# Kernel tuning notes

Measured on AMD Instinct MI355X. Metric: run time of the kernel, lower is better.

The kernel has to match this reference:

```python
import jax, jax.numpy as jnp
import numpy as np

T, N, D, L, H = 128, 256, 256, 3, 4


def _ln(x, s, b):
    m = jnp.mean(x, axis=-1, keepdims=True)
    v = jnp.mean((x - m) ** 2, axis=-1, keepdims=True)
    return (x - m) / jnp.sqrt(v + 1e-5) * s + b


def setup_inputs() -> dict:
    key = jax.random.key(0)
    ks = jax.random.split(key, 12)
    s = 0.05
    d = D
    return {
        "spatial_states": jax.random.normal(ks[0], (T, N, d), jnp.float32),
        "re_norm": jax.random.uniform(ks[1], (), jnp.float32),
        "sensor_time": jnp.cumsum(jax.random.uniform(ks[2], (T,), jnp.float32) * 0.1),
        "re_proj_w": jax.random.normal(ks[3], (d, 1), jnp.float32) * s,
        "re_proj_b": jnp.zeros((d,), jnp.float32),
        "tb_n1_s": jnp.ones((d,), jnp.float32),
        "tb_n1_b": jnp.zeros((d,), jnp.float32),
        "tb_in_w": jax.random.normal(ks[4], (3 * d, d), jnp.float32) * s,
        "tb_in_b": jnp.zeros((3 * d,), jnp.float32),
        "tb_out_w": jax.random.normal(ks[5], (d, d), jnp.float32) * s,
        "tb_out_b": jnp.zeros((d,), jnp.float32),
        "tb_n2_s": jnp.ones((d,), jnp.float32),
        "tb_n2_b": jnp.zeros((d,), jnp.float32),
        "tb_ff1_w": jax.random.normal(ks[6], (2 * d, d), jnp.float32) * s,
        "tb_ff1_b": jnp.zeros((2 * d,), jnp.float32),
        "tb_ff2_w": jax.random.normal(ks[7], (d, 2 * d), jnp.float32) * s,
        "tb_ff2_b": jnp.zeros((d,), jnp.float32),
        "cell_ff1_w": jax.random.normal(ks[8], (L, d, 2 * d), jnp.float32) * s,
        "cell_ff1_b": jnp.zeros((L, d), jnp.float32),
        "cell_ff2_w": jax.random.normal(ks[9], (L, d, 2 * d), jnp.float32) * s,
        "cell_ff2_b": jnp.zeros((L, d), jnp.float32),
        "cell_logtau": jnp.tile(jnp.linspace(-1.0, 1.0, d, dtype=jnp.float32), (L, 1)),
        "cell_tb_w": jax.random.normal(ks[10], (L, d, 2 * d), jnp.float32) * s,
        "cell_tb_b": jnp.zeros((L, d), jnp.float32),
    }


def reference(spatial_states, re_norm, sensor_time,
              re_proj_w, re_proj_b,
              tb_n1_s, tb_n1_b, tb_in_w, tb_in_b, tb_out_w, tb_out_b,
              tb_n2_s, tb_n2_b, tb_ff1_w, tb_ff1_b, tb_ff2_w, tb_ff2_b,
              cell_ff1_w, cell_ff1_b, cell_ff2_w, cell_ff2_b,
              cell_logtau, cell_tb_w, cell_tb_b):
    t, n, d = spatial_states.shape
    nL = cell_logtau.shape[0]
    hd = d // H

    # dt per step: first absolute time, then diffs (as in torch source)
    dts = jnp.concatenate([sensor_time[:1], sensor_time[1:] - sensor_time[:-1]])  # [T]
    re_bias = re_proj_w[:, 0] * re_norm + re_proj_b  # [d]

    def token_block(x):  # x: [T, N, d]; attention over N, batched over T
        y = _ln(x, tb_n1_s, tb_n1_b)
        qkv = y @ tb_in_w.T + tb_in_b
        q, k, v = jnp.split(qkv, 3, axis=-1)
        q = q.reshape(t, n, H, hd)
        k = k.reshape(t, n, H, hd)
        v = v.reshape(t, n, H, hd)
        logits = jnp.einsum('bqhd,bkhd->bhqk', q, k) / jnp.sqrt(jnp.float32(hd))
        a = jax.nn.softmax(logits, axis=-1)
        o = jnp.einsum('bhqk,bkhd->bqhd', a, v).reshape(t, n, d)
        x = x + (o @ tb_out_w.T + tb_out_b)
        y = _ln(x, tb_n2_s, tb_n2_b)
        f = jax.nn.silu(y @ tb_ff1_w.T + tb_ff1_b) @ tb_ff2_w.T + tb_ff2_b
        return x + f

    seq = spatial_states
    for l in range(nL):
        # token attention + re_bias are independent of the recurrence -> vectorize over T
        xs = token_block(seq) + re_bias  # [T, N, d]
        w1, b1 = cell_ff1_w[l], cell_ff1_b[l]
        w2, b2 = cell_ff2_w[l], cell_ff2_b[l]
        wt, bt = cell_tb_w[l], cell_tb_b[l]
        tau = jnp.exp(cell_logtau[l])  # [d]

        def step(h, xd):
            x_t, dt = xd
            xh = jnp.concatenate([x_t, h], axis=-1)  # [N, 2d]
            f1 = jnp.tanh(xh @ w1.T + b1)
            f2 = jnp.tanh(xh @ w2.T + b2)
            gate = jax.nn.sigmoid(-tau * dt + (xh @ wt.T + bt))
            h_new = gate * f1 + (1.0 - gate) * f2
            return h_new, h_new

        h0 = jnp.zeros((n, d), seq.dtype)
        _, outs = jax.lax.scan(step, h0, (xs, dts))  # outs: [T, N, d]
        seq = outs + seq if l > 0 else outs
    return seq
```

## Files before the change

kernel.cpp:

```cpp
#include <hip/hip_runtime.h>


#define T_DIM 128
#define N_DIM 256
#define D_DIM 256
#define H_DIM 4
#define HD_DIM 64
#define L_DIM 3
#define TN (T_DIM * N_DIM)

typedef __bf16 bf16x8 __attribute__((ext_vector_type(8)));
typedef __bf16 bf16x4 __attribute__((ext_vector_type(4)));
typedef float f32x4 __attribute__((ext_vector_type(4)));

#define LDS_BAR()                                            \
  do {                                                       \
    asm volatile("s_waitcnt lgkmcnt(0)" ::: "memory");       \
    __builtin_amdgcn_s_barrier();                            \
    __builtin_amdgcn_sched_barrier(0);                       \
  } while (0)

__device__ inline float wave_reduce_sum(float v) {
#pragma unroll
  for (int off = 32; off > 0; off >>= 1) v += __shfl_xor(v, off);
  return v;
}

__device__ inline float bf_to_f(unsigned short u) {
  return __uint_as_float((unsigned int)u << 16);
}

__global__ __launch_bounds__(256) void ln_kernel(const float* __restrict__ x,
                                                 const float* __restrict__ sc,
                                                 const float* __restrict__ bi,
                                                 __bf16* __restrict__ y) {
  const int wid = threadIdx.x >> 6;
  const int lane = threadIdx.x & 63;
  const size_t row = (size_t)blockIdx.x * 4 + wid;
  const float4 xv = *(const float4*)(x + row * D_DIM + lane * 4);
  float s = xv.x + xv.y + xv.z + xv.w;
  float ss = xv.x * xv.x + xv.y * xv.y + xv.z * xv.z + xv.w * xv.w;
  s = wave_reduce_sum(s);
  ss = wave_reduce_sum(ss);
  const float mean = s * (1.f / D_DIM);
  const float var = ss * (1.f / D_DIM) - mean * mean;
  const float r = rsqrtf(var + 1e-5f);
  const float4 scv = *(const float4*)(sc + lane * 4);
  const float4 biv = *(const float4*)(bi + lane * 4);
  bf16x4 ov;
  ov[0] = (__bf16)((xv.x - mean) * r * scv.x + biv.x);
  ov[1] = (__bf16)((xv.y - mean) * r * scv.y + biv.y);
  ov[2] = (__bf16)((xv.z - mean) * r * scv.z + biv.z);
  ov[3] = (__bf16)((xv.w - mean) * r * scv.w + biv.w);
  *(bf16x4*)(y + row * D_DIM + lane * 4) = ov;
}

template <int EPI, int OBF>
__global__ __launch_bounds__(256) void gemm_tiled(const __bf16* __restrict__ A,
                                                  const __bf16* __restrict__ W,
                                                  const float* __restrict__ bias,
                                                  const float* __restrict__ R,
                                                  void* __restrict__ outv,
                                                  int M, int Nout, int K) {
  __shared__ __bf16 a_lds[128][72];
  __shared__ __bf16 b_lds[128][72];
  const int tid = threadIdx.x;
  const int w = tid >> 6, l = tid & 63;
  const int lr = l & 15, kg = l >> 4;
  const int wm = (w & 1) * 64, wn = (w >> 1) * 64;
  const int m0 = blockIdx.x * 128, n0 = blockIdx.y * 128;
  const int srow = tid >> 1, scol = (tid & 1) * 32;
  const __bf16* ag = A + (size_t)(m0 + srow) * K + scol;
  const __bf16* bg = W + (size_t)(n0 + srow) * K + scol;

  bf16x8 av[4], bv[4];
#pragma unroll
  for (int c = 0; c < 4; ++c) {
    av[c] = *(const bf16x8*)(ag + c * 8);
    bv[c] = *(const bf16x8*)(bg + c * 8);
  }

  f32x4 acc[4][4] = {};
  for (int k0 = 0; k0 < K; k0 += 64) {
    LDS_BAR();
#pragma unroll
    for (int c = 0; c < 4; ++c) {
      *(bf16x8*)&a_lds[srow][scol + c * 8] = av[c];
      *(bf16x8*)&b_lds[srow][scol + c * 8] = bv[c];
    }
    if (k0 + 64 < K) {
#pragma unroll
      for (int c = 0; c < 4; ++c) {
        av[c] = *(const bf16x8*)(ag + k0 + 64 + c * 8);
        bv[c] = *(const bf16x8*)(bg + k0 + 64 + c * 8);
      }
    }
    LDS_BAR();
#pragma unroll
    for (int ks = 0; ks < 2; ++ks) {
      bf16x8 af[4], bf[4];
#pragma unroll
      for (int mt = 0; mt < 4; ++mt)
        af[mt] = *(const bf16x8*)&a_lds[wm + mt * 16 + lr][ks * 32 + kg * 8];
#pragma unroll
      for (int nt = 0; nt < 4; ++nt)
        bf[nt] = *(const bf16x8*)&b_lds[wn + nt * 16 + lr][ks * 32 + kg * 8];
#pragma unroll
      for (int mt = 0; mt < 4; ++mt)
#pragma unroll
        for (int nt = 0; nt < 4; ++nt)
          acc[mt][nt] =
              __builtin_amdgcn_mfma_f32_16x16x32_bf16(af[mt], bf[nt], acc[mt][nt], 0, 0, 0);
    }
  }
#pragma unroll
  for (int nt = 0; nt < 4; ++nt) {
    const int col = n0 + wn + nt * 16 + lr;
    const float bvs = bias[col];
#pragma unroll
    for (int mt = 0; mt < 4; ++mt) {
#pragma unroll
      for (int j = 0; j < 4; ++j) {
        const int row = m0 + wm + mt * 16 + kg * 4 + j;
        float v = acc[mt][nt][j] + bvs;
        if (EPI == 1) v += R[(size_t)row * Nout + col];
        if (EPI == 2) v = v * (1.f / (1.f + __expf(-v)));
        const size_t oi = (size_t)row * Nout + col;
        if (OBF)
          ((__bf16*)outv)[oi] = (__bf16)v;
        else
          ((float*)outv)[oi] = v;
      }
    }
  }
}

__global__ __launch_bounds__(256, 2) void attn_mfma(const __bf16* __restrict__ qkv,
                                                    __bf16* __restrict__ o) {
  const int t = blockIdx.x, h = blockIdx.y;
  const int tid = threadIdx.x;
  const int w = tid >> 6, l = tid & 63;
  const int lr = l & 15, kg = l >> 4;

  __shared__ __bf16 vt_lds[64 * 256];
  __shared__ __bf16 p_lds[4][16 * 256];

  {
    const __bf16* vrow = qkv + ((size_t)(t * N_DIM + tid)) * 768 + 512 + h * HD_DIM;
#pragma unroll
    for (int c8 = 0; c8 < 64; c8 += 8) {
      bf16x8 v = *(const bf16x8*)(vrow + c8);
#pragma unroll
      for (int i = 0; i < 8; ++i) {
        const int c = c8 + i;
        const int byte = (c * 512 + tid * 2) ^ ((c & 7) << 4);
        *(__bf16*)((char*)vt_lds + byte) = v[i];
      }
    }
  }
  __syncthreads();

  const __bf16* kbase = qkv + (size_t)t * N_DIM * 768 + 256 + h * HD_DIM;
  const __bf16* qbase = qkv + (size_t)t * N_DIM * 768 + h * HD_DIM;
  char* pw = (char*)&p_lds[w][0];

  for (int qt = 0; qt < 4; ++qt) {
    const int q0 = w * 64 + qt * 16;
    const bf16x8 qf0 = *(const bf16x8*)(qbase + (size_t)(q0 + lr) * 768 + kg * 8);
    const bf16x8 qf1 = *(const bf16x8*)(qbase + (size_t)(q0 + lr) * 768 + 32 + kg * 8);
    f32x4 acc[16];
#pragma unroll
    for (int nt = 0; nt < 16; ++nt) {
      const bf16x8 a0 = *(const bf16x8*)(kbase + (size_t)(nt * 16 + lr) * 768 + kg * 8);
      const bf16x8 a1 = *(const bf16x8*)(kbase + (size_t)(nt * 16 + lr) * 768 + 32 + kg * 8);
      f32x4 s = {};
      s = __builtin_amdgcn_mfma_f32_16x16x32_bf16(a0, qf0, s, 0, 0, 0);
      s = __builtin_amdgcn_mfma_f32_16x16x32_bf16(a1, qf1, s, 0, 0, 0);
      acc[nt] = s;
    }
    float mx = -3.0e38f;
#pragma unroll
    for (int nt = 0; nt < 16; ++nt)
#pragma unroll
      for (int j = 0; j < 4; ++j) mx = fmaxf(mx, acc[nt][j]);
    mx = fmaxf(mx, __shfl_xor(mx, 16));
    mx = fmaxf(mx, __shfl_xor(mx, 32));
    float sum = 0.f;
#pragma unroll
    for (int nt = 0; nt < 16; ++nt) {
      bf16x4 pb;
#pragma unroll
      for (int j = 0; j < 4; ++j) {
        const float p = __expf((acc[nt][j] - mx) * 0.125f);
        pb[j] = (__bf16)p;
        sum += (float)pb[j];
      }
      const int byte = (lr * 512 + nt * 32 + kg * 8) ^ ((lr & 7) << 4);
      *(bf16x4*)(pw + byte) = pb;
    }
    sum += __shfl_xor(sum, 16);
    sum += __shfl_xor(sum, 32);
    const float inv = 1.f / sum;
    f32x4 oacc[4] = {};
#pragma unroll
    for (int kt = 0; kt < 8; ++kt) {
      const int pbyte = (lr * 512 + kt * 64 + kg * 16) ^ ((lr & 7) << 4);
      const bf16x8 bfrag = *(const bf16x8*)(pw + pbyte);
#pragma unroll
      for (int ct = 0; ct < 4; ++ct) {
        const int c = ct * 16 + lr;
        const int vbyte = (c * 512 + kt * 64 + kg * 16) ^ ((c & 7) << 4);
        const bf16x8 afrag = *(const bf16x8*)((char*)vt_lds + vbyte);
        oacc[ct] = __builtin_amdgcn_mfma_f32_16x16x32_bf16(afrag, bfrag, oacc[ct], 0, 0, 0);
      }
    }
    __bf16* orow = o + ((size_t)(t * N_DIM + q0 + lr)) * D_DIM + h * HD_DIM;
#pragma unroll
    for (int ct = 0; ct < 4; ++ct) {
      bf16x4 ov;
#pragma unroll
      for (int j = 0; j < 4; ++j) ov[j] = (__bf16)(oacc[ct][j] * inv);
      *(bf16x4*)(orow + ct * 16 + kg * 4) = ov;
    }
  }
}

__global__ __launch_bounds__(256, 1) void scan_mfma(const __bf16* __restrict__ P,
                                                    const __bf16* __restrict__ Wh,
                                                    const float* __restrict__ logtau,
                                                    const float* __restrict__ st,
                                                    const float* __restrict__ addsrc,
                                                    float* __restrict__ out) {
  const int tid = threadIdx.x;
  const int w = tid >> 6, l = tid & 63;
  const int lr = l & 15, kg = l >> 4;
  const int n = blockIdx.x;

  __shared__ float acc2[776];
  __shared__ __bf16 h_lds[264];
  __shared__ float dts[T_DIM];

  if (tid < T_DIM) dts[tid] = (tid == 0) ? st[0] : st[tid] - st[tid - 1];
  if (tid < 33) ((bf16x8*)h_lds)[tid] = (bf16x8){};

  bf16x8 wreg[12][8];
  {
    const __bf16* wb = Wh + (size_t)(w * 192 + lr) * 256 + kg * 8;
#pragma unroll
    for (int nt = 0; nt < 12; ++nt)
#pragma unroll
      for (int kt = 0; kt < 8; ++kt)
        wreg[nt][kt] = *(const bf16x8*)(wb + (size_t)nt * 16 * 256 + kt * 32);
  }
  __syncthreads();

  const int d = tid;
  const float tau = __expf(logtau[d]);
  const unsigned short* Pp = (const unsigned short*)P + (size_t)n * 768 + d;
  float* op = out + (size_t)n * D_DIM + d;
  const float* ap = addsrc ? addsrc + (size_t)n * D_DIM + d : nullptr;
  const char* hbase = (const char*)h_lds + kg * 16;

  unsigned short c1 = Pp[0], c2 = Pp[256], c3 = Pp[512];
  unsigned short n1 = 0, n2 = 0, n3 = 0;
  {
    const unsigned short* Pn = Pp + (size_t)N_DIM * 768;
    n1 = Pn[0]; n2 = Pn[256]; n3 = Pn[512];
  }
  float av = ap ? ap[0] : 0.f;
  float nav = ap ? ap[(size_t)N_DIM * D_DIM] : 0.f;

  for (int t = 0; t < T_DIM; ++t) {
    unsigned short m1 = 0, m2 = 0, m3 = 0;
    float mav = 0.f;
    if (t + 2 < T_DIM) {
      const unsigned short* Pm = Pp + (size_t)(t + 2) * N_DIM * 768;
      m1 = Pm[0]; m2 = Pm[256]; m3 = Pm[512];
      if (ap) mav = ap[(size_t)(t + 2) * N_DIM * D_DIM];
    }

    f32x4 acc[12] = {};
#pragma unroll
    for (int kt = 0; kt < 8; ++kt) {
      const bf16x8 a = *(const bf16x8*)(hbase + kt * 64);
#pragma unroll
      for (int nt = 0; nt < 12; ++nt)
        acc[nt] = __builtin_amdgcn_mfma_f32_16x16x32_bf16(a, wreg[nt][kt], acc[nt], 0, 0, 0);
    }
    if (l < 16) {
#pragma unroll
      for (int nt = 0; nt < 12; ++nt) acc2[w * 192 + nt * 16 + lr] = acc[nt][0];
    }
    LDS_BAR();

    const float dt = dts[t];
    const float a1 = acc2[d] + bf_to_f(c1);
    const float a2 = acc2[256 + d] + bf_to_f(c2);
    const float a3 = acc2[512 + d] + bf_to_f(c3) - tau * dt;
    const float e1 = __expf(-2.f * fabsf(a1));
    const float f1 = copysignf((1.f - e1) / (1.f + e1), a1);
    const float e2 = __expf(-2.f * fabsf(a2));
    const float f2 = copysignf((1.f - e2) / (1.f + e2), a2);
    const float g = 1.f / (1.f + __expf(-a3));
    const float hn = g * f1 + (1.f - g) * f2;
    h_lds[d] = (__bf16)hn;
    op[(size_t)t * N_DIM * D_DIM] = hn + av;
    LDS_BAR();

    c1 = n1; c2 = n2; c3 = n3; av = nav;
    n1 = m1; n2 = m2; n3 = m3; nav = mav;
  }
}

__global__ void cvt_kernel(const float* __restrict__ src, __bf16* __restrict__ dst, int n) {
  const int i = blockIdx.x * 256 + threadIdx.x;
  if (i < n) dst[i] = (__bf16)src[i];
}

__global__ void pack_cell_kernel(const float* __restrict__ w1, const float* __restrict__ w2,
                                 const float* __restrict__ wt, __bf16* __restrict__ Wx,
                                 __bf16* __restrict__ Whb) {
  const int idx = blockIdx.x * 256 + threadIdx.x;
  if (idx >= 3 * 768 * 256) return;
  const int l = idx / (768 * 256);
  const int r2 = idx - l * (768 * 256);
  const int jj = r2 >> 8;
  const int c = r2 & 255;
  const int m = jj >> 8;
  const int r = jj & 255;
  const float* src = (m == 0 ? w1 : (m == 1 ? w2 : wt)) + ((size_t)l * 256 + r) * 512;
  Wx[(size_t)l * (768 * 256) + (size_t)jj * 256 + c] = (__bf16)src[c];
  Whb[(size_t)l * (768 * 256) + (size_t)jj * 256 + c] = (__bf16)src[256 + c];
}

__global__ void bias_pack_kernel(const float* __restrict__ b1, const float* __restrict__ b2,
                                 const float* __restrict__ bt, const float* __restrict__ ff2b,
                                 const float* __restrict__ rw, const float* __restrict__ rb,
                                 const float* __restrict__ rn, float* __restrict__ bias768,
                                 float* __restrict__ ff2bias) {
  const int idx = blockIdx.x * 256 + threadIdx.x;
  if (idx < 3 * 768) {
    const int l = idx / 768, jj = idx % 768, m = jj >> 8, r = jj & 255;
    const float* s = (m == 0 ? b1 : (m == 1 ? b2 : bt));
    bias768[idx] = s[l * 256 + r];
  }
  if (idx < 256) ff2bias[idx] = ff2b[idx] + rw[idx] * rn[0] + rb[idx];
}

extern "C" void kernel_launch(void* const* d_in, const int* in_sizes, int n_in,
                              void* d_out, int out_size, void* d_ws, size_t ws_size,
                              hipStream_t stream) {
  (void)in_sizes; (void)n_in; (void)out_size; (void)ws_size;
  const float* spatial = (const float*)d_in[0];
  const float* re_norm = (const float*)d_in[1];
  const float* sensor_time = (const float*)d_in[2];
  const float* re_proj_w = (const float*)d_in[3];
  const float* re_proj_b = (const float*)d_in[4];
  const float* n1s = (const float*)d_in[5];
  const float* n1b = (const float*)d_in[6];
  const float* in_w = (const float*)d_in[7];
  const float* in_b = (const float*)d_in[8];
  const float* out_w = (const float*)d_in[9];
  const float* out_b = (const float*)d_in[10];
  const float* n2s = (const float*)d_in[11];
  const float* n2b = (const float*)d_in[12];
  const float* ff1_w = (const float*)d_in[13];
  const float* ff1_b = (const float*)d_in[14];
  const float* ff2_w = (const float*)d_in[15];
  const float* ff2_b = (const float*)d_in[16];
  const float* c1w = (const float*)d_in[17];
  const float* c1b = (const float*)d_in[18];
  const float* c2w = (const float*)d_in[19];
  const float* c2b = (const float*)d_in[20];
  const float* clt = (const float*)d_in[21];
  const float* ctw = (const float*)d_in[22];
  const float* ctb = (const float*)d_in[23];

  char* ws = (char*)d_ws;
  size_t off = 0;
  auto alloc = [&](size_t b) {
    char* p = ws + off;
    off = (off + b + 255) & ~(size_t)255;
    return p;
  };
  float* seq = (float*)alloc((size_t)TN * D_DIM * 4);
  float* xb = (float*)alloc((size_t)TN * D_DIM * 4);
  __bf16* yb = (__bf16*)alloc((size_t)TN * D_DIM * 2);
  char* big = (char*)alloc((size_t)TN * 768 * 2);
  __bf16* qkvb = (__bf16*)big;
  __bf16* gb = (__bf16*)big;
  __bf16* Pb = (__bf16*)big;
  __bf16* w_in = (__bf16*)alloc(768 * 256 * 2);
  __bf16* w_out = (__bf16*)alloc(256 * 256 * 2);
  __bf16* w_f1 = (__bf16*)alloc(512 * 256 * 2);
  __bf16* w_f2 = (__bf16*)alloc(256 * 512 * 2);
  __bf16* Wx = (__bf16*)alloc((size_t)3 * 768 * 256 * 2);
  __bf16* Whb = (__bf16*)alloc((size_t)3 * 768 * 256 * 2);
  float* b768 = (float*)alloc(3 * 768 * 4);
  float* f2bias = (float*)alloc(256 * 4);

  cvt_kernel<<<(768 * 256 + 255) / 256, 256, 0, stream>>>(in_w, w_in, 768 * 256);
  cvt_kernel<<<(256 * 256 + 255) / 256, 256, 0, stream>>>(out_w, w_out, 256 * 256);
  cvt_kernel<<<(512 * 256 + 255) / 256, 256, 0, stream>>>(ff1_w, w_f1, 512 * 256);
  cvt_kernel<<<(256 * 512 + 255) / 256, 256, 0, stream>>>(ff2_w, w_f2, 256 * 512);
  pack_cell_kernel<<<(3 * 768 * 256 + 255) / 256, 256, 0, stream>>>(c1w, c2w, ctw, Wx, Whb);
  bias_pack_kernel<<<9, 256, 0, stream>>>(c1b, c2b, ctb, ff2_b, re_proj_w, re_proj_b,
                                          re_norm, b768, f2bias);

  for (int l = 0; l < L_DIM; ++l) {
    const float* seq_in = (l == 0) ? spatial : seq;
    ln_kernel<<<TN / 4, 256, 0, stream>>>(seq_in, n1s, n1b, yb);
    gemm_tiled<0, 1><<<dim3(TN / 128, 768 / 128), 256, 0, stream>>>(yb, w_in, in_b, nullptr,
                                                                    qkvb, TN, 768, 256);
    attn_mfma<<<dim3(T_DIM, H_DIM), 256, 0, stream>>>(qkvb, yb);
    gemm_tiled<1, 0><<<dim3(TN / 128, 256 / 128), 256, 0, stream>>>(yb, w_out, out_b, seq_in,
                                                                    xb, TN, 256, 256);
    ln_kernel<<<TN / 4, 256, 0, stream>>>(xb, n2s, n2b, yb);
    gemm_tiled<2, 1><<<dim3(TN / 128, 512 / 128), 256, 0, stream>>>(yb, w_f1, ff1_b, nullptr,
                                                                    gb, TN, 512, 256);
    gemm_tiled<1, 1><<<dim3(TN / 128, 256 / 128), 256, 0, stream>>>(gb, w_f2, f2bias, xb, yb,
                                                                    TN, 256, 512);
    gemm_tiled<0, 1><<<dim3(TN / 128, 768 / 128), 256, 0, stream>>>(
        yb, Wx + (size_t)l * 768 * 256, b768 + l * 768, nullptr, Pb, TN, 768, 256);
    float* outp = (l == 2) ? (float*)d_out : seq;
    const float* addp = (l == 0) ? nullptr : seq;
    scan_mfma<<<N_DIM, 256, 0, stream>>>(Pb, Whb + (size_t)l * 768 * 256,
                                         clt + l * 256, sensor_time, addp, outp);
  }
}
```

Baseline: 1.337 ms.

## Replace MFMA recurrent scan with per-thread fp16 dot2 and double-buffered state

The recurrent scan drops the 16x16 MFMA tiles, where only one row of each tile is useful, along with their LDS staging of partial sums. Each thread now computes its own three gate pre-activations with fp16 fdot2 over weights held in registers. The hidden state is double-buffered in LDS, so each step needs one barrier instead of two. The costs are 384 packed weight registers per thread, which risks spills or AGPR use, and many more VALU dot instructions per step. Recurrent weights and state also switch from bf16 to fp16.

Result: slower. 1.593 ms (+19.2%).

```diff
diff --git a/kernel.cpp b/kernel.cpp
--- a/kernel.cpp
+++ b/kernel.cpp
@@ -12,6 +12,7 @@
 typedef __bf16 bf16x8 __attribute__((ext_vector_type(8)));
 typedef __bf16 bf16x4 __attribute__((ext_vector_type(4)));
 typedef float f32x4 __attribute__((ext_vector_type(4)));
+typedef _Float16 f16x2 __attribute__((ext_vector_type(2)));
 
 #define LDS_BAR()                                            \
   do {                                                       \
@@ -225,85 +226,96 @@
   }
 }
 
-__global__ __launch_bounds__(256, 1) void scan_mfma(const __bf16* __restrict__ P,
-                                                    const __bf16* __restrict__ Wh,
-                                                    const float* __restrict__ logtau,
-                                                    const float* __restrict__ st,
-                                                    const float* __restrict__ addsrc,
-                                                    float* __restrict__ out) {
+__global__ __launch_bounds__(256, 1) void scan_dot(const __bf16* __restrict__ P,
+                                                   const _Float16* __restrict__ Whf,
+                                                   const float* __restrict__ logtau,
+                                                   const float* __restrict__ st,
+                                                   const float* __restrict__ addsrc,
+                                                   float* __restrict__ out) {
   const int tid = threadIdx.x;
-  const int w = tid >> 6, l = tid & 63;
-  const int lr = l & 15, kg = l >> 4;
   const int n = blockIdx.x;
 
-  __shared__ float acc2[776];
-  __shared__ __bf16 h_lds[264];
+  __shared__ _Float16 h_buf[2][264];
   __shared__ float dts[T_DIM];
 
   if (tid < T_DIM) dts[tid] = (tid == 0) ? st[0] : st[tid] - st[tid - 1];
-  if (tid < 33) ((bf16x8*)h_lds)[tid] = (bf16x8){};
-
-  bf16x8 wreg[12][8];
+  if (tid < 33) {
+    *(uint4*)&h_buf[0][tid * 8] = (uint4){0, 0, 0, 0};
+    *(uint4*)&h_buf[1][tid * 8] = (uint4){0, 0, 0, 0};
+  }
+
+  f16x2 w1[128], w2[128], w3[128];
   {
-    const __bf16* wb = Wh + (size_t)(w * 192 + lr) * 256 + kg * 8;
-#pragma unroll
-    for (int nt = 0; nt < 12; ++nt)
-#pragma unroll
-      for (int kt = 0; kt < 8; ++kt)
-        wreg[nt][kt] = *(const bf16x8*)(wb + (size_t)nt * 16 * 256 + kt * 32);
-  }
-  __syncthreads();
-
-  const int d = tid;
-  const float tau = __expf(logtau[d]);
-  const unsigned short* Pp = (const unsigned short*)P + (size_t)n * 768 + d;
-  float* op = out + (size_t)n * D_DIM + d;
-  const float* ap = addsrc ? addsrc + (size_t)n * D_DIM + d : nullptr;
-  const char* hbase = (const char*)h_lds + kg * 16;
+    const f16x2* p1 = (const f16x2*)(Whf + (size_t)tid * 256);
+    const f16x2* p2 = (const f16x2*)(Whf + (size_t)(256 + tid) * 256);
+    const f16x2* p3 = (const f16x2*)(Whf + (size_t)(512 + tid) * 256);
+#pragma unroll
+    for (int i = 0; i < 128; ++i) {
+      w1[i] = p1[i];
+      w2[i] = p2[i];
+      w3[i] = p3[i];
+    }
+  }
+  const float tau = __expf(logtau[tid]);
+
+  const unsigned short* Pp = (const unsigned short*)P + (size_t)n * 768 + tid;
+  float* op = out + (size_t)n * D_DIM + tid;
+  const float* ap = addsrc ? addsrc + (size_t)n * D_DIM + tid : nullptr;
 
   unsigned short c1 = Pp[0], c2 = Pp[256], c3 = Pp[512];
-  unsigned short n1 = 0, n2 = 0, n3 = 0;
-  {
-    const unsigned short* Pn = Pp + (size_t)N_DIM * 768;
-    n1 = Pn[0]; n2 = Pn[256]; n3 = Pn[512];
-  }
+  const unsigned short* Pn = Pp + (size_t)N_DIM * 768;
+  unsigned short n1 = Pn[0], n2 = Pn[256], n3 = Pn[512];
   float av = ap ? ap[0] : 0.f;
   float nav = ap ? ap[(size_t)N_DIM * D_DIM] : 0.f;
+
+  __syncthreads();
 
   for (int t = 0; t < T_DIM; ++t) {
     unsigned short m1 = 0, m2 = 0, m3 = 0;
     float mav = 0.f;
     if (t + 2 < T_DIM) {
       const unsigned short* Pm = Pp + (size_t)(t + 2) * N_DIM * 768;
-      m1 = Pm[0]; m2 = Pm[256]; m3 = Pm[512];
+      m1 = Pm[0];
+      m2 = Pm[256];
+      m3 = Pm[512];
       if (ap) mav = ap[(size_t)(t + 2) * N_DIM * D_DIM];
     }
 
-    f32x4 acc[12] = {};
-#pragma unroll
-    for (int kt = 0; kt < 8; ++kt) {
-      const bf16x8 a = *(const bf16x8*)(hbase + kt * 64);
-#pragma unroll
-      for (int nt = 0; nt < 12; ++nt)
-        acc[nt] = __builtin_amdgcn_mfma_f32_16x16x32_bf16(a, wreg[nt][kt], acc[nt], 0, 0, 0);
-    }
-    if (l < 16) {
-#pragma unroll
-      for (int nt = 0; nt < 12; ++nt) acc2[w * 192 + nt * 16 + lr] = acc[nt][0];
-    }
-    LDS_BAR();
+    const _Float16* hb = &h_buf[t & 1][0];
+    float a1 = 0.f, a2 = 0.f, a3 = 0.f;
+#pragma unroll
+    for (int c = 0; c < 32; ++c) {
+      const uint4 hu = *(const uint4*)(hb + c * 8);
+      const f16x2 h0 = __builtin_bit_cast(f16x2, hu.x);
+      const f16x2 h1 = __builtin_bit_cast(f16x2, hu.y);
+      const f16x2 h2 = __builtin_bit_cast(f16x2, hu.z);
+      const f16x2 h3 = __builtin_bit_cast(f16x2, hu.w);
+      a1 = __builtin_amdgcn_fdot2(h0, w1[c * 4 + 0], a1, false);
+      a2 = __builtin_amdgcn_fdot2(h0, w2[c * 4 + 0], a2, false);
+      a3 = __builtin_amdgcn_fdot2(h0, w3[c * 4 + 0], a3, false);
+      a1 = __builtin_amdgcn_fdot2(h1, w1[c * 4 + 1], a1, false);
+      a2 = __builtin_amdgcn_fdot2(h1, w2[c * 4 + 1], a2, false);
+      a3 = __builtin_amdgcn_fdot2(h1, w3[c * 4 + 1], a3, false);
+      a1 = __builtin_amdgcn_fdot2(h2, w1[c * 4 + 2], a1, false);
+      a2 = __builtin_amdgcn_fdot2(h2, w2[c * 4 + 2], a2, false);
+      a3 = __builtin_amdgcn_fdot2(h2, w3[c * 4 + 2], a3, false);
+      a1 = __builtin_amdgcn_fdot2(h3, w1[c * 4 + 3], a1, false);
+      a2 = __builtin_amdgcn_fdot2(h3, w2[c * 4 + 3], a2, false);
+      a3 = __builtin_amdgcn_fdot2(h3, w3[c * 4 + 3], a3, false);
+    }
 
     const float dt = dts[t];
-    const float a1 = acc2[d] + bf_to_f(c1);
-    const float a2 = acc2[256 + d] + bf_to_f(c2);
-    const float a3 = acc2[512 + d] + bf_to_f(c3) - tau * dt;
-    const float e1 = __expf(-2.f * fabsf(a1));
-    const float f1 = copysignf((1.f - e1) / (1.f + e1), a1);
-    const float e2 = __expf(-2.f * fabsf(a2));
-    const float f2 = copysignf((1.f - e2) / (1.f + e2), a2);
-    const float g = 1.f / (1.f + __expf(-a3));
+    const float A1 = a1 + bf_to_f(c1);
+    const float A2 = a2 + bf_to_f(c2);
+    const float A3 = a3 + bf_to_f(c3) - tau * dt;
+    const float e1 = __expf(-2.f * fabsf(A1));
+    const float f1 = copysignf((1.f - e1) / (1.f + e1), A1);
+    const float e2 = __expf(-2.f * fabsf(A2));
+    const float f2 = copysignf((1.f - e2) / (1.f + e2), A2);
+    const float g = 1.f / (1.f + __expf(-A3));
     const float hn = g * f1 + (1.f - g) * f2;
-    h_lds[d] = (__bf16)hn;
+
+    h_buf[(t + 1) & 1][tid] = (_Float16)hn;
     op[(size_t)t * N_DIM * D_DIM] = hn + av;
     LDS_BAR();
 
@@ -319,7 +331,7 @@
 
 __global__ void pack_cell_kernel(const float* __restrict__ w1, const float* __restrict__ w2,
                                  const float* __restrict__ wt, __bf16* __restrict__ Wx,
-                                 __bf16* __restrict__ Whb) {
+                                 _Float16* __restrict__ Whf) {
   const int idx = blockIdx.x * 256 + threadIdx.x;
   if (idx >= 3 * 768 * 256) return;
   const int l = idx / (768 * 256);
@@ -330,7 +342,7 @@
   const int r = jj & 255;
   const float* src = (m == 0 ? w1 : (m == 1 ? w2 : wt)) + ((size_t)l * 256 + r) * 512;
   Wx[(size_t)l * (768 * 256) + (size_t)jj * 256 + c] = (__bf16)src[c];
-  Whb[(size_t)l * (768 * 256) + (size_t)jj * 256 + c] = (__bf16)src[256 + c];
+  Whf[(size_t)l * (768 * 256) + (size_t)jj * 256 + c] = (_Float16)src[256 + c];
 }
 
 __global__ void bias_pack_kernel(const float* __restrict__ b1, const float* __restrict__ b2,
@@ -395,7 +407,7 @@
   __bf16* w_f1 = (__bf16*)alloc(512 * 256 * 2);
   __bf16* w_f2 = (__bf16*)alloc(256 * 512 * 2);
   __bf16* Wx = (__bf16*)alloc((size_t)3 * 768 * 256 * 2);
-  __bf16* Whb = (__bf16*)alloc((size_t)3 * 768 * 256 * 2);
+  _Float16* Whf = (_Float16*)alloc((size_t)3 * 768 * 256 * 2);
   float* b768 = (float*)alloc(3 * 768 * 4);
   float* f2bias = (float*)alloc(256 * 4);
 
@@ -403,7 +415,7 @@
   cvt_kernel<<<(256 * 256 + 255) / 256, 256, 0, stream>>>(out_w, w_out, 256 * 256);
   cvt_kernel<<<(512 * 256 + 255) / 256, 256, 0, stream>>>(ff1_w, w_f1, 512 * 256);
   cvt_kernel<<<(256 * 512 + 255) / 256, 256, 0, stream>>>(ff2_w, w_f2, 256 * 512);
-  pack_cell_kernel<<<(3 * 768 * 256 + 255) / 256, 256, 0, stream>>>(c1w, c2w, ctw, Wx, Whb);
+  pack_cell_kernel<<<(3 * 768 * 256 + 255) / 256, 256, 0, stream>>>(c1w, c2w, ctw, Wx, Whf);
   bias_pack_kernel<<<9, 256, 0, stream>>>(c1b, c2b, ctb, ff2_b, re_proj_w, re_proj_b,
                                           re_norm, b768, f2bias);
 
@@ -424,7 +436,7 @@
         yb, Wx + (size_t)l * 768 * 256, b768 + l * 768, nullptr, Pb, TN, 768, 256);
     float* outp = (l == 2) ? (float*)d_out : seq;
     const float* addp = (l == 0) ? nullptr : seq;
-    scan_mfma<<<N_DIM, 256, 0, stream>>>(Pb, Whb + (size_t)l * 768 * 256,
-                                         clt + l * 256, sensor_time, addp, outp);
-  }
-}
+    scan_dot<<<N_DIM, 256, 0, stream>>>(Pb, Whf + (size_t)l * 768 * 256, clt + l * 256,
+                                        sensor_time, addp, outp);
+  }
+}
```
